# Kernel optimization log

Hardware: AMD Instinct MI355X
Metric: run time of the kernel (lower is better)

Reference implementation:

```python
import jax, jax.numpy as jnp
import numpy as np

N_USER = 50000
N_ITEM = 100000
D = 64            # embed_size; layer_size = [64, 64, 64]
NL = 3            # number of propagation layers
NNZ = 2400000     # nonzeros of sparse Laplacian L
B = 1024          # batch of (user, pos_item, neg_item)
N = N_USER + N_ITEM


def setup_inputs() -> dict:
    key = jax.random.key(0)
    ks = jax.random.split(key, 20)
    inp = {}
    # learned parameters
    inp["user_emb"] = jax.random.normal(ks[0], (N_USER, D), jnp.float32) * 0.1
    inp["item_emb"] = jax.random.normal(ks[1], (N_ITEM, D), jnp.float32) * 0.1
    inp["lin1_w"] = jax.random.normal(ks[2], (4, D // 2), jnp.float32) * 0.5
    inp["lin1_b"] = jnp.zeros((D // 2,), jnp.float32)
    inp["lin2_w"] = jax.random.normal(ks[3], (D // 2, D), jnp.float32) * 0.2
    inp["lin2_b"] = jnp.zeros((D,), jnp.float32)
    inp["w1"] = jax.random.normal(ks[4], (NL, D, D), jnp.float32) * (1.0 / np.sqrt(D))
    inp["b1"] = jnp.zeros((NL, D), jnp.float32)
    inp["w2"] = jax.random.normal(ks[5], (NL, D, D), jnp.float32) * (1.0 / np.sqrt(D))
    inp["b2"] = jnp.zeros((NL, D), jnp.float32)
    # sparse normalized Laplacian L in COO form (eye_mat handled as +E)
    inp["lap_row"] = jax.random.randint(ks[6], (NNZ,), 0, N, jnp.int32)
    inp["lap_col"] = jax.random.randint(ks[7], (NNZ,), 0, N, jnp.int32)
    inp["lap_val"] = jax.random.uniform(ks[8], (NNZ,), jnp.float32) * (1.0 / 16.0)
    # forward args
    inp["user_idx"] = jax.random.randint(ks[9], (B,), 0, N_USER, jnp.int32)
    inp["user_feat"] = jax.random.normal(ks[10], (B, 4), jnp.float32)
    inp["pos_idx"] = jax.random.randint(ks[11], (B,), 0, N_ITEM, jnp.int32)
    inp["neg_idx"] = jax.random.randint(ks[12], (B,), 0, N_ITEM, jnp.int32)
    inp["mlp_ratio"] = jnp.float32(0.5)
    return inp


def reference(user_emb, item_emb, user_feat, lin1_w, lin1_b, lin2_w, lin2_b,
              w1, b1, w2, b2, lap_val, mlp_ratio,
              lap_row, lap_col, user_idx, pos_idx, neg_idx):
    n_user = user_emb.shape[0]
    n_nodes = user_emb.shape[0] + item_emb.shape[0]

    # user MLP: two stacked Linears (no activation in between, per Sequential)
    user_mlp = (user_feat @ lin1_w + lin1_b) @ lin2_w + lin2_b  # [B, D]
    # in-place no_grad embedding blend (stop_gradient mirrors torch.no_grad on mlp path)
    upd = user_emb[user_idx] * (1.0 - mlp_ratio) + jax.lax.stop_gradient(user_mlp) * mlp_ratio
    ue = user_emb.at[user_idx].set(upd)

    E = jnp.concatenate([ue, item_emb], axis=0)  # [N, D]

    def spmm(X):
        # L @ X via gather-multiply-segment_sum over COO nonzeros
        return jax.ops.segment_sum(lap_val[:, None] * X[lap_col], lap_row,
                                   num_segments=n_nodes)

    all_E = [E]
    for k in range(w1.shape[0]):
        L_E = spmm(E)                 # L @ E
        L_I_E = L_E + E               # (L + I) @ E
        msg = (L_I_E @ w1[k] + b1[k]) + ((L_E * E) @ w2[k] + b2[k])
        E = jax.nn.leaky_relu(msg, negative_slope=0.2)
        # F.normalize(E, p=2, dim=1) with eps=1e-12
        norm = E / jnp.maximum(jnp.linalg.norm(E, axis=1, keepdims=True), 1e-12)
        all_E.append(norm)

    all_E = jnp.concatenate(all_E, axis=1)  # [N, D*(NL+1)]
    users = all_E[:n_user]
    items = all_E[n_user:]
    return (users[user_idx], items[pos_idx], items[neg_idx])
```

## Files before the change

kernel.cpp:

```cpp
#include <hip/hip_runtime.h>
#include <hip/hip_bf16.h>

#define N_USERC 50000
#define N_ITEMC 100000
#define NNODE   150000
#define DIM     64
#define NLAYERS 3
#define NNZC    2400000
#define BATCH   1024

#define RPB     128
#define NBUCK   1172
#define NCHUNK  512
#define CHUNK   4688
#define CAPB    3072
#define NPARTB  8

using short8 = __attribute__((ext_vector_type(8))) short;
using f32x4  = __attribute__((ext_vector_type(4))) float;
using uintx4 = __attribute__((ext_vector_type(4))) unsigned;

__device__ __forceinline__ float bf2f(ushort u) {
    return __uint_as_float(((unsigned)u) << 16);
}
__device__ __forceinline__ ushort f2bf(float f) {
    unsigned u = __float_as_uint(f);
    u += 0x7FFF + ((u >> 16) & 1);
    return (ushort)(u >> 16);
}

__device__ __forceinline__ int block_excl_scan(int v, int* lds) {
    int lane = threadIdx.x & 63;
    int wid  = threadIdx.x >> 6;
    int nw   = (blockDim.x + 63) >> 6;
    int inc = v;
#pragma unroll
    for (int o = 1; o < 64; o <<= 1) {
        int n = __shfl_up(inc, o, 64);
        if (lane >= o) inc += n;
    }
    if (lane == 63) lds[wid] = inc;
    __syncthreads();
    if (wid == 0) {
        int tv = (lane < nw) ? lds[lane] : 0;
#pragma unroll
        for (int o = 1; o < 16; o <<= 1) {
            int n = __shfl_up(tv, o, 64);
            if (lane >= o) tv += n;
        }
        if (lane < nw) lds[lane] = tv;
    }
    __syncthreads();
    int woff = (wid == 0) ? 0 : lds[wid - 1];
    return woff + (inc - v);
}

__global__ __launch_bounds__(256) void k_prep(const float* __restrict__ ue,
                                              const float* __restrict__ ie,
                                              ushort* __restrict__ Ebf,
                                              const float* __restrict__ w1,
                                              const float* __restrict__ w2,
                                              ushort* __restrict__ Wtg,
                                              const int* __restrict__ user_idx,
                                              int* __restrict__ winner) {
    int i = blockIdx.x * blockDim.x + threadIdx.x;
    const int userEnd = N_USERC * DIM / 4;
    const int total   = NNODE * DIM / 4;
    if (i < total) {
        float4 v;
        if (i < userEnd) v = ((const float4*)ue)[i];
        else             v = ((const float4*)ie)[i - userEnd];
        ushort4 b;
        b.x = f2bf(v.x); b.y = f2bf(v.y); b.z = f2bf(v.z); b.w = f2bf(v.w);
        ((ushort4*)Ebf)[i] = b;
    }
    if (i < NLAYERS * 64 * 128) {
        int layer = i >> 13;
        int rem = i & 8191;
        int n = rem >> 7, kk = rem & 127;
        float v = (kk < 64) ? w1[layer * 4096 + kk * 64 + n]
                            : w2[layer * 4096 + (kk - 64) * 64 + n];
        Wtg[i] = f2bf(v);
    }
    if (i < BATCH) atomicMax(&winner[user_idx[i]], i);
}

__global__ void k_mlp_update(const float* __restrict__ user_emb,
                             const float* __restrict__ user_feat,
                             const float* __restrict__ l1w, const float* __restrict__ l1b,
                             const float* __restrict__ l2w, const float* __restrict__ l2b,
                             const float* __restrict__ ratio_p,
                             const int* __restrict__ user_idx,
                             const int* __restrict__ winner,
                             ushort* __restrict__ Ebf) {
    int b = blockIdx.x;
    int d = threadIdx.x;
    int u = user_idx[b];
    if (winner[u] != b) return;
    float ratio = ratio_p[0];
    float uf0 = user_feat[b * 4 + 0], uf1 = user_feat[b * 4 + 1];
    float uf2 = user_feat[b * 4 + 2], uf3 = user_feat[b * 4 + 3];
    float acc = l2b[d];
#pragma unroll
    for (int j = 0; j < 32; ++j) {
        float h = l1b[j] + uf0 * l1w[0 * 32 + j] + uf1 * l1w[1 * 32 + j]
                         + uf2 * l1w[2 * 32 + j] + uf3 * l1w[3 * 32 + j];
        acc += h * l2w[j * DIM + d];
    }
    float v = user_emb[u * DIM + d] * (1.f - ratio) + acc * ratio;
    Ebf[u * DIM + d] = f2bf(v);
}

__global__ __launch_bounds__(256) void k_chunksort(const int* __restrict__ rows,
                                                   const int* __restrict__ cols,
                                                   const float* __restrict__ vals,
                                                   unsigned long long* __restrict__ tmp,
                                                   ushort* __restrict__ scanus,
                                                   int* __restrict__ winner) {
    __shared__ int hist[NBUCK];
    __shared__ int sutil[16];
    __shared__ unsigned long long stag[CHUNK];

    const int c = blockIdx.x;
    const int s = c * CHUNK;
    const int e = (s + CHUNK < NNZC) ? s + CHUNK : NNZC;
    const int t = threadIdx.x;

    for (int i = c * 256 + t; i < N_USERC; i += NCHUNK * 256) winner[i] = -1;

    for (int i = t; i < NBUCK; i += 256) hist[i] = 0;
    __syncthreads();
    for (int i = s + t; i < e; i += 256) atomicAdd(&hist[rows[i] >> 7], 1);
    __syncthreads();

    int loc[5];
    int sum = 0;
#pragma unroll
    for (int k = 0; k < 5; ++k) {
        int idx = t * 5 + k;
        int v = (idx < NBUCK) ? hist[idx] : 0;
        loc[k] = sum;
        sum += v;
    }
    int excl = block_excl_scan(sum, sutil);
#pragma unroll
    for (int k = 0; k < 5; ++k) {
        int idx = t * 5 + k;
        if (idx < NBUCK) hist[idx] = excl + loc[k];
    }
    __syncthreads();

    for (int i = t; i < NBUCK; i += 256) scanus[(size_t)c * (NBUCK + 1) + i] = (ushort)hist[i];
    if (t == 0) scanus[(size_t)c * (NBUCK + 1) + NBUCK] = (ushort)(e - s);
    __syncthreads();

    for (int i = s + t; i < e; i += 256) {
        int r = rows[i];
        int b = r >> 7, ro = r & 127;
        unsigned hi = ((unsigned)ro << 18) | (unsigned)cols[i];
        unsigned long long pk = ((unsigned long long)hi << 32) | (unsigned)__float_as_uint(vals[i]);
        int pos = atomicAdd(&hist[b], 1);
        stag[pos] = pk;
    }
    __syncthreads();

    int n = e - s;
    for (int i = t; i < n; i += 256) tmp[s + i] = stag[i];
}

__global__ __launch_bounds__(256) void k_buckcnt(const ushort* __restrict__ scanus,
                                                 int* __restrict__ bcntp) {
    int b = blockIdx.x * 256 + threadIdx.x;
    int g = blockIdx.y;
    if (b >= NBUCK) return;
    int c0 = g * (NCHUNK / NPARTB), c1 = c0 + NCHUNK / NPARTB;
    int sum = 0;
    for (int c = c0; c < c1; ++c) {
        const ushort* row = scanus + (size_t)c * (NBUCK + 1);
        sum += (int)row[b + 1] - (int)row[b];
    }
    bcntp[g * NBUCK + b] = sum;
}

__global__ __launch_bounds__(256) void k_bscan(const int* __restrict__ bcntp,
                                               int* __restrict__ bstart,
                                               int* __restrict__ rowptr) {
    __shared__ int sutil[16];
    int t = threadIdx.x;
    int loc[5];
    int sum = 0;
#pragma unroll
    for (int k = 0; k < 5; ++k) {
        int idx = t * 5 + k;
        int v = 0;
        if (idx < NBUCK) {
#pragma unroll
            for (int g = 0; g < NPARTB; ++g) v += bcntp[g * NBUCK + idx];
        }
        loc[k] = sum;
        sum += v;
    }
    int excl = block_excl_scan(sum, sutil);
#pragma unroll
    for (int k = 0; k < 5; ++k) {
        int idx = t * 5 + k;
        if (idx < NBUCK) bstart[idx] = excl + loc[k];
    }
    if (t == 0) { bstart[NBUCK] = NNZC; rowptr[NNODE] = NNZC; }
}

__global__ __launch_bounds__(256) void k_compact(const ushort* __restrict__ scanus,
                                                 const int* __restrict__ bstart,
                                                 const unsigned long long* __restrict__ tmp,
                                                 unsigned long long* __restrict__ csr,
                                                 int* __restrict__ rowptr) {
    __shared__ int runstart[NCHUNK];
    __shared__ int pref[NCHUNK + 1];
    __shared__ int sutil[16];
    __shared__ int rcur[RPB];
    __shared__ unsigned long long stag[CAPB];
    const int b = blockIdx.x;
    const int t = threadIdx.x;

    for (int r = t; r < NCHUNK; r += 256) {
        const ushort* row = scanus + (size_t)r * (NBUCK + 1);
        int s0 = row[b], s1 = row[b + 1];
        runstart[r] = r * CHUNK + s0;
        pref[r] = s1 - s0;
    }
    if (t < RPB) rcur[t] = 0;
    __syncthreads();
    int v0 = pref[t * 2], v1 = pref[t * 2 + 1];
    int sum = v0 + v1;
    int excl = block_excl_scan(sum, sutil);
    pref[t * 2] = excl;
    pref[t * 2 + 1] = excl + v0;
    if (t == 255) pref[NCHUNK] = excl + sum;
    __syncthreads();

    const int total = pref[NCHUNK];
    const int obase = bstart[b];

    if (total <= CAPB) {
        for (int r = t; r < NCHUNK; r += 256) {
            int p0 = pref[r], p1 = pref[r + 1];
            int rs = runstart[r];
            for (int i = p0; i < p1; ++i) stag[i] = tmp[rs + (i - p0)];
        }
        __syncthreads();
        for (int i = t; i < total; i += 256)
            atomicAdd(&rcur[(int)(stag[i] >> 50) & 127], 1);
        __syncthreads();
        int rv = (t < RPB) ? rcur[t] : 0;
        int rex = block_excl_scan(rv, sutil);
        if (t < RPB) {
            rcur[t] = rex;
            int grow = b * RPB + t;
            if (grow < NNODE) rowptr[grow] = obase + rex;
        }
        __syncthreads();
        for (int i = t; i < total; i += 256) {
            unsigned long long pk = stag[i];
            int ro = (int)(pk >> 50) & 127;
            int pos = atomicAdd(&rcur[ro], 1);
            csr[obase + pos] = pk;
        }
        return;
    }

    for (int i = t; i < total; i += 256) {
        int lo = 0, hi = NCHUNK - 1;
        while (lo < hi) {
            int mid = (lo + hi + 1) >> 1;
            if (pref[mid] <= i) lo = mid; else hi = mid - 1;
        }
        unsigned long long pk = tmp[runstart[lo] + (i - pref[lo])];
        atomicAdd(&rcur[(int)(pk >> 50) & 127], 1);
    }
    __syncthreads();
    int rv = (t < RPB) ? rcur[t] : 0;
    int rex = block_excl_scan(rv, sutil);
    if (t < RPB) {
        rcur[t] = rex;
        int grow = b * RPB + t;
        if (grow < NNODE) rowptr[grow] = obase + rex;
    }
    __syncthreads();
    for (int i = t; i < total; i += 256) {
        int lo = 0, hi = NCHUNK - 1;
        while (lo < hi) {
            int mid = (lo + hi + 1) >> 1;
            if (pref[mid] <= i) lo = mid; else hi = mid - 1;
        }
        unsigned long long pk = tmp[runstart[lo] + (i - pref[lo])];
        int ro = (int)(pk >> 50) & 127;
        int pos = atomicAdd(&rcur[ro], 1);
        csr[obase + pos] = pk;
    }
}

__global__ __launch_bounds__(256) void k_spmm(const int* __restrict__ rowptr,
                                              const unsigned long long* __restrict__ csr,
                                              const ushort* __restrict__ Ebf,
                                              ushort* __restrict__ Abf) {
    int lane = threadIdx.x & 63;
    int row  = blockIdx.x * 4 + (threadIdx.x >> 6);
    row = __builtin_amdgcn_readfirstlane(row);
    if (row >= NNODE) return;
    int s = __builtin_amdgcn_readfirstlane(rowptr[row]);
    int e = __builtin_amdgcn_readfirstlane(rowptr[row + 1]);
    const ushort* Ep = Ebf + lane;
    float eo = bf2f(Ebf[row * DIM + lane]);
    float acc = 0.f;
    int j = s;
    for (; j + 16 <= e; j += 16) {
        unsigned long long pk[16];
        float ev[16];
#pragma unroll
        for (int k = 0; k < 16; ++k) pk[k] = csr[j + k];
#pragma unroll
        for (int k = 0; k < 16; ++k) {
            int col = (int)(pk[k] >> 32) & 0x3FFFF;
            ev[k] = bf2f(Ep[col * DIM]);
        }
#pragma unroll
        for (int k = 0; k < 16; ++k)
            acc += __uint_as_float((unsigned)pk[k]) * ev[k];
    }
    if (j < e) {
        int m = e - j;
        unsigned long long pk[16];
        float ev[16];
#pragma unroll
        for (int k = 0; k < 16; ++k) pk[k] = csr[j + k];
#pragma unroll
        for (int k = 0; k < 16; ++k) {
            int col = (k < m) ? ((int)(pk[k] >> 32) & 0x3FFFF) : 0;
            ev[k] = bf2f(Ep[col * DIM]);
        }
#pragma unroll
        for (int k = 0; k < 16; ++k) {
            unsigned v = (k < m) ? (unsigned)pk[k] : 0u;
            acc += __uint_as_float(v) * ev[k];
        }
    }
    __builtin_nontemporal_store(f2bf(acc + eo), &Abf[row * 128 + lane]);
    __builtin_nontemporal_store(f2bf(acc * eo), &Abf[row * 128 + 64 + lane]);
}

__global__ __launch_bounds__(256) void k_transform(const ushort* __restrict__ Abf,
                                                   const ushort* __restrict__ Wtg,
                                                   const float* __restrict__ b1k,
                                                   const float* __restrict__ b2k,
                                                   ushort* __restrict__ Ebf_out) {
    __shared__ ushort A_s[64 * 136];
    __shared__ ushort W_s[64 * 136];
    __shared__ float  bias_s[64];

    const int t = threadIdx.x;
    const int rowbase = blockIdx.x * 64;
    if (t < 64) bias_s[t] = b1k[t] + b2k[t];

#pragma unroll
    for (int it = 0; it < 4; ++it) {
        int task = t + 256 * it;
        int n = task >> 4, k = (task & 15) * 8;
        uint4 wv = *(const uint4*)&Wtg[n * 128 + k];
        *(uint4*)&W_s[n * 136 + k] = wv;
    }
#pragma unroll
    for (int it = 0; it < 4; ++it) {
        int task = t + 256 * it;
        int rl = task >> 4, k8 = (task & 15) * 8;
        int row = rowbase + rl;
        uintx4 v = {0u, 0u, 0u, 0u};
        if (row < NNODE)
            v = __builtin_nontemporal_load((const uintx4*)&Abf[row * 128 + k8]);
        *(uintx4*)&A_s[rl * 136 + k8] = v;
    }
    __syncthreads();

    const int w = t >> 6, l = t & 63;
    const int m16 = l & 15;
    const int q   = l >> 4;
    const int lm  = w * 16 + m16;

    f32x4 z = {0.f, 0.f, 0.f, 0.f};
    f32x4 acc[4] = {z, z, z, z};
#pragma unroll
    for (int ks = 0; ks < 4; ++ks) {
        short8 af = *(const short8*)&A_s[lm * 136 + ks * 32 + q * 8];
#pragma unroll
        for (int nt = 0; nt < 4; ++nt) {
            short8 wf = *(const short8*)&W_s[(nt * 16 + m16) * 136 + ks * 32 + q * 8];
            acc[nt] = __builtin_amdgcn_mfma_f32_16x16x32_bf16(af, wf, acc[nt], 0, 0, 0);
        }
    }
    __syncthreads();

    float* Cs = (float*)A_s;
#pragma unroll
    for (int nt = 0; nt < 4; ++nt) {
        int col = nt * 16 + m16;
#pragma unroll
        for (int r = 0; r < 4; ++r) {
            int lrow = w * 16 + q * 4 + r;
            Cs[lrow * 68 + col] = acc[nt][r];
        }
    }
    __syncthreads();

#pragma unroll
    for (int it = 0; it < 2; ++it) {
        int task = t + 256 * it;
        int rl = task >> 3, col = (task & 7) * 8;
        int row = rowbase + rl;
        if (row < NNODE) {
            float4 v0 = *(const float4*)&Cs[rl * 68 + col];
            float4 v1 = *(const float4*)&Cs[rl * 68 + col + 4];
            float o[8] = {v0.x, v0.y, v0.z, v0.w, v1.x, v1.y, v1.z, v1.w};
            ushort ob[8];
#pragma unroll
            for (int j = 0; j < 8; ++j) {
                float v = o[j] + bias_s[col + j];
                v = v >= 0.f ? v : 0.2f * v;
                ob[j] = f2bf(v);
            }
            uint4 pb;
            pb.x = (unsigned)ob[0] | ((unsigned)ob[1] << 16);
            pb.y = (unsigned)ob[2] | ((unsigned)ob[3] << 16);
            pb.z = (unsigned)ob[4] | ((unsigned)ob[5] << 16);
            pb.w = (unsigned)ob[6] | ((unsigned)ob[7] << 16);
            *(uint4*)&Ebf_out[row * 64 + col] = pb;
        }
    }
}

__global__ __launch_bounds__(256) void k_gather(const ushort* __restrict__ Ebf,
                                                const int* __restrict__ user_idx,
                                                const int* __restrict__ pos_idx,
                                                const int* __restrict__ neg_idx,
                                                float* __restrict__ out,
                                                int seg, int normalize) {
    int wid  = threadIdx.x >> 6;
    int lane = threadIdx.x & 63;
    int o = blockIdx.x * 4 + wid;
    if (o >= 3 * BATCH) return;
    int g = o >> 10, b = o & 1023;
    int row;
    if (g == 0)      row = user_idx[b];
    else if (g == 1) row = N_USERC + pos_idx[b];
    else             row = N_USERC + neg_idx[b];
    float v = bf2f(Ebf[row * DIM + lane]);
    if (normalize) {
        float ss = v * v;
#pragma unroll
        for (int m = 32; m; m >>= 1) ss += __shfl_xor(ss, m, 64);
        float nrm = sqrtf(ss);
        nrm = fmaxf(nrm, 1e-12f);
        v = v / nrm;
    }
    out[(g * BATCH + b) * 256 + seg * 64 + lane] = v;
}

extern "C" void kernel_launch(void* const* d_in, const int* in_sizes, int n_in,
                              void* d_out, int out_size, void* d_ws, size_t ws_size,
                              hipStream_t stream) {
    const float* user_emb  = (const float*)d_in[0];
    const float* item_emb  = (const float*)d_in[1];
    const float* lin1_w    = (const float*)d_in[2];
    const float* lin1_b    = (const float*)d_in[3];
    const float* lin2_w    = (const float*)d_in[4];
    const float* lin2_b    = (const float*)d_in[5];
    const float* w1        = (const float*)d_in[6];
    const float* b1        = (const float*)d_in[7];
    const float* w2        = (const float*)d_in[8];
    const float* b2        = (const float*)d_in[9];
    const int*   lap_row   = (const int*)d_in[10];
    const int*   lap_col   = (const int*)d_in[11];
    const float* lap_val   = (const float*)d_in[12];
    const int*   user_idx  = (const int*)d_in[13];
    const float* user_feat = (const float*)d_in[14];
    const int*   pos_idx   = (const int*)d_in[15];
    const int*   neg_idx   = (const int*)d_in[16];
    const float* mlp_ratio = (const float*)d_in[17];
    float* out = (float*)d_out;

    size_t off = 0;
    auto carve = [&](size_t bytes) { size_t r = off; off = (off + bytes + 255) & ~(size_t)255; return r; };
    size_t oL      = carve((size_t)NNODE * DIM * 4);
    size_t oEbf    = carve((size_t)NNODE * DIM * 2);
    size_t oCsr    = carve((size_t)NNZC * 8);
    size_t oScan   = carve((size_t)NCHUNK * (NBUCK + 1) * 2);
    size_t oBcnt   = carve((size_t)NBUCK * 4);
    size_t oBstart = carve((size_t)(NBUCK + 1) * 4);
    size_t oRowptr = carve((size_t)(NNODE + 1) * 4);
    size_t oWinner = carve((size_t)N_USERC * 4);
    size_t oBcntP  = carve((size_t)NPARTB * NBUCK * 4);
    (void)ws_size; (void)oBcnt;

    char* base = (char*)d_ws;
    ushort*             Abf    = (ushort*)(base + oL);
    unsigned long long* tmp    = (unsigned long long*)(base + oL);
    ushort*             Ebf    = (ushort*)(base + oEbf);
    unsigned long long* csr    = (unsigned long long*)(base + oCsr);
    ushort*             scanus = (ushort*)(base + oScan);
    int*                bstart = (int*)(base + oBstart);
    int*                rowptr = (int*)(base + oRowptr);
    int*                winner = (int*)(base + oWinner);
    int*                bcntp  = (int*)(base + oBcntP);
    ushort*             Wtg    = (ushort*)(base + oScan);

    k_chunksort<<<NCHUNK, 256, 0, stream>>>(lap_row, lap_col, lap_val, tmp, scanus, winner);
    k_buckcnt<<<dim3(5, NPARTB), 256, 0, stream>>>(scanus, bcntp);
    k_bscan<<<1, 256, 0, stream>>>(bcntp, bstart, rowptr);
    k_compact<<<NBUCK, 256, 0, stream>>>(scanus, bstart, tmp, csr, rowptr);

    k_prep<<<(NNODE * DIM / 4 + 255) / 256, 256, 0, stream>>>(
        user_emb, item_emb, Ebf, w1, w2, Wtg, user_idx, winner);
    k_mlp_update<<<BATCH, 64, 0, stream>>>(user_emb, user_feat, lin1_w, lin1_b,
                                           lin2_w, lin2_b, mlp_ratio, user_idx, winner, Ebf);
    k_gather<<<(3 * BATCH) / 4, 256, 0, stream>>>(Ebf, user_idx, pos_idx, neg_idx, out, 0, 0);

    for (int k = 0; k < NLAYERS; ++k) {
        k_spmm<<<(NNODE + 3) / 4, 256, 0, stream>>>(rowptr, csr, Ebf, Abf);
        k_transform<<<(NNODE + 63) / 64, 256, 0, stream>>>(
            Abf, Wtg + (size_t)k * 64 * 128, b1 + (size_t)k * DIM,
            b2 + (size_t)k * DIM, Ebf);
        k_gather<<<(3 * BATCH) / 4, 256, 0, stream>>>(Ebf, user_idx, pos_idx, neg_idx,
                                                      out, k + 1, 1);
    }
}
```

Before: 419.0 us.

## Transpose chunk scan table and compute bucket starts by summing per-chunk prefixes

Each chunk's bucket offset table is now stored bucket-major instead of chunk-major. This lets one wavefront sum a bucket's exclusive offsets across all chunks with coalesced vector loads. Summing per-chunk exclusive prefixes gives the global bucket start directly, so the separate count kernel and the single-block scan kernel merge into one small kernel. The cost is that the sort kernel now writes the table with a strided, uncoalesced pattern, while the compact kernel's reads become coalesced.

```diff
diff --git a/kernel.cpp b/kernel.cpp
--- a/kernel.cpp
+++ b/kernel.cpp
@@ -17,6 +17,7 @@
 #define NPARTB  8
 
 using short8 = __attribute__((ext_vector_type(8))) short;
+using us8    = __attribute__((ext_vector_type(8))) unsigned short;
 using f32x4  = __attribute__((ext_vector_type(4))) float;
 using uintx4 = __attribute__((ext_vector_type(4))) unsigned;
 
@@ -115,7 +116,7 @@
                                                    const int* __restrict__ cols,
                                                    const float* __restrict__ vals,
                                                    unsigned long long* __restrict__ tmp,
-                                                   ushort* __restrict__ scanus,
+                                                   ushort* __restrict__ scanT,
                                                    int* __restrict__ winner) {
     __shared__ int hist[NBUCK];
     __shared__ int sutil[16];
@@ -150,8 +151,8 @@
     }
     __syncthreads();
 
-    for (int i = t; i < NBUCK; i += 256) scanus[(size_t)c * (NBUCK + 1) + i] = (ushort)hist[i];
-    if (t == 0) scanus[(size_t)c * (NBUCK + 1) + NBUCK] = (ushort)(e - s);
+    for (int i = t; i < NBUCK; i += 256) scanT[(size_t)i * NCHUNK + c] = (ushort)hist[i];
+    if (t == 0) scanT[(size_t)NBUCK * NCHUNK + c] = (ushort)(e - s);
     __syncthreads();
 
     for (int i = s + t; i < e; i += 256) {
@@ -168,48 +169,26 @@
     for (int i = t; i < n; i += 256) tmp[s + i] = stag[i];
 }
 
-__global__ __launch_bounds__(256) void k_buckcnt(const ushort* __restrict__ scanus,
-                                                 int* __restrict__ bcntp) {
-    int b = blockIdx.x * 256 + threadIdx.x;
-    int g = blockIdx.y;
+__global__ __launch_bounds__(256) void k_buckcnt(const ushort* __restrict__ scanT,
+                                                 int* __restrict__ bstart,
+                                                 int* __restrict__ rowptr) {
+    int wid  = threadIdx.x >> 6;
+    int lane = threadIdx.x & 63;
+    int b = blockIdx.x * 4 + wid;
+    if (blockIdx.x == 0 && threadIdx.x == 0) {
+        bstart[NBUCK] = NNZC;
+        rowptr[NNODE] = NNZC;
+    }
     if (b >= NBUCK) return;
-    int c0 = g * (NCHUNK / NPARTB), c1 = c0 + NCHUNK / NPARTB;
-    int sum = 0;
-    for (int c = c0; c < c1; ++c) {
-        const ushort* row = scanus + (size_t)c * (NBUCK + 1);
-        sum += (int)row[b + 1] - (int)row[b];
-    }
-    bcntp[g * NBUCK + b] = sum;
-}
-
-__global__ __launch_bounds__(256) void k_bscan(const int* __restrict__ bcntp,
-                                               int* __restrict__ bstart,
-                                               int* __restrict__ rowptr) {
-    __shared__ int sutil[16];
-    int t = threadIdx.x;
-    int loc[5];
-    int sum = 0;
-#pragma unroll
-    for (int k = 0; k < 5; ++k) {
-        int idx = t * 5 + k;
-        int v = 0;
-        if (idx < NBUCK) {
-#pragma unroll
-            for (int g = 0; g < NPARTB; ++g) v += bcntp[g * NBUCK + idx];
-        }
-        loc[k] = sum;
-        sum += v;
-    }
-    int excl = block_excl_scan(sum, sutil);
-#pragma unroll
-    for (int k = 0; k < 5; ++k) {
-        int idx = t * 5 + k;
-        if (idx < NBUCK) bstart[idx] = excl + loc[k];
-    }
-    if (t == 0) { bstart[NBUCK] = NNZC; rowptr[NNODE] = NNZC; }
-}
-
-__global__ __launch_bounds__(256) void k_compact(const ushort* __restrict__ scanus,
+    us8 v = *(const us8*)&scanT[(size_t)b * NCHUNK + lane * 8];
+    int ss = (int)v[0] + (int)v[1] + (int)v[2] + (int)v[3]
+           + (int)v[4] + (int)v[5] + (int)v[6] + (int)v[7];
+#pragma unroll
+    for (int m = 32; m; m >>= 1) ss += __shfl_xor(ss, m, 64);
+    if (lane == 0) bstart[b] = ss;
+}
+
+__global__ __launch_bounds__(256) void k_compact(const ushort* __restrict__ scanT,
                                                  const int* __restrict__ bstart,
                                                  const unsigned long long* __restrict__ tmp,
                                                  unsigned long long* __restrict__ csr,
@@ -223,8 +202,8 @@
     const int t = threadIdx.x;
 
     for (int r = t; r < NCHUNK; r += 256) {
-        const ushort* row = scanus + (size_t)r * (NBUCK + 1);
-        int s0 = row[b], s1 = row[b + 1];
+        int s0 = scanT[(size_t)b * NCHUNK + r];
+        int s1 = scanT[(size_t)(b + 1) * NCHUNK + r];
         runstart[r] = r * CHUNK + s0;
         pref[r] = s1 - s0;
     }
@@ -497,24 +476,22 @@
     size_t oRowptr = carve((size_t)(NNODE + 1) * 4);
     size_t oWinner = carve((size_t)N_USERC * 4);
     size_t oBcntP  = carve((size_t)NPARTB * NBUCK * 4);
-    (void)ws_size; (void)oBcnt;
+    (void)ws_size; (void)oBcnt; (void)oBcntP;
 
     char* base = (char*)d_ws;
     ushort*             Abf    = (ushort*)(base + oL);
     unsigned long long* tmp    = (unsigned long long*)(base + oL);
     ushort*             Ebf    = (ushort*)(base + oEbf);
     unsigned long long* csr    = (unsigned long long*)(base + oCsr);
-    ushort*             scanus = (ushort*)(base + oScan);
+    ushort*             scanT  = (ushort*)(base + oScan);
     int*                bstart = (int*)(base + oBstart);
     int*                rowptr = (int*)(base + oRowptr);
     int*                winner = (int*)(base + oWinner);
-    int*                bcntp  = (int*)(base + oBcntP);
     ushort*             Wtg    = (ushort*)(base + oScan);
 
-    k_chunksort<<<NCHUNK, 256, 0, stream>>>(lap_row, lap_col, lap_val, tmp, scanus, winner);
-    k_buckcnt<<<dim3(5, NPARTB), 256, 0, stream>>>(scanus, bcntp);
-    k_bscan<<<1, 256, 0, stream>>>(bcntp, bstart, rowptr);
-    k_compact<<<NBUCK, 256, 0, stream>>>(scanus, bstart, tmp, csr, rowptr);
+    k_chunksort<<<NCHUNK, 256, 0, stream>>>(lap_row, lap_col, lap_val, tmp, scanT, winner);
+    k_buckcnt<<<(NBUCK + 3) / 4, 256, 0, stream>>>(scanT, bstart, rowptr);
+    k_compact<<<NBUCK, 256, 0, stream>>>(scanT, bstart, tmp, csr, rowptr);
 
     k_prep<<<(NNODE * DIM / 4 + 255) / 256, 256, 0, stream>>>(
         user_emb, item_emb, Ebf, w1, w2, Wtg, user_idx, winner);
```

Measured after the change: 417.1 us. No clear change (-0.5%).
